# Kernel tuning notes

Measured on AMD Instinct MI355X. Metric: run time of the kernel, lower is better.

The kernel has to match this reference:

```python
import jax, jax.numpy as jnp
import numpy as np

N = 2048          # nodes
IN_DIM = 512      # in_dim
H = 8             # num_heads
HD = IN_DIM // H  # head_dim = 64
L = 5             # max_path_len
E = 32768         # edges
D_EDGE = 64       # edge_feat_dim


def setup_inputs() -> dict:
    key = jax.random.key(0)
    ks = jax.random.split(key, 14)
    w = 1.0 / np.sqrt(IN_DIM)
    return {
        "node_feat": jax.random.normal(ks[0], (N, IN_DIM), jnp.float32),
        "edge_index": jax.random.randint(ks[1], (2, E), 0, N, dtype=jnp.int32),
        "max_path_len": 5,
        "shortest_distances": jax.random.randint(ks[2], (N, N), 0, L + 1, dtype=jnp.int32),
        "shortest_paths": jax.random.randint(ks[3], (N, N, L), 0, E + 1, dtype=jnp.int32),  # E == padding row
        "edge_feat": jax.random.normal(ks[4], (E, D_EDGE), jnp.float32),
        "attention_mask": jnp.zeros((N, N), jnp.int32),
        "WQ": jax.random.normal(ks[5], (IN_DIM, IN_DIM), jnp.float32) * w,
        "bQ": jax.random.normal(ks[6], (IN_DIM,), jnp.float32) * 0.02,
        "WK": jax.random.normal(ks[7], (IN_DIM, IN_DIM), jnp.float32) * w,
        "bK": jax.random.normal(ks[8], (IN_DIM,), jnp.float32) * 0.02,
        "WV": jax.random.normal(ks[9], (IN_DIM, IN_DIM), jnp.float32) * w,
        "bV": jax.random.normal(ks[10], (IN_DIM,), jnp.float32) * 0.02,
        "WO": jax.random.normal(ks[11], (IN_DIM, IN_DIM), jnp.float32) * w,
        "bO": jnp.zeros((IN_DIM,), jnp.float32),
        "spatial_bias": jax.random.normal(ks[12], ((L + 1) * H, 1), jnp.float32) * 0.02,
        "edge_weight": jax.random.normal(ks[13], ((L + 1) * H, D_EDGE), jnp.float32) * 0.02,
    }


def reference(node_feat, edge_index, max_path_len, shortest_distances, shortest_paths,
              edge_feat, attention_mask, WQ, bQ, WK, bK, WV, bV, WO, bO,
              spatial_bias, edge_weight):
    Nn, D = node_feat.shape
    Lp = max_path_len  # min(max_path_len, max_shortest_path_len); distances reach Lp here

    Q = (node_feat @ WQ + bQ).reshape(Nn, H, HD)
    K = (node_feat @ WK + bK).reshape(Nn, H, HD)
    V = (node_feat @ WV + bV).reshape(Nn, H, HD)

    # QK^T / sqrt(head_dim), laid out [N, N, H] as in the original after permute
    scores = jnp.einsum('nhd,mhd->nmh', Q, K) / np.sqrt(HD).astype(np.float32)

    # SpatialEncoding: bias table [(L+1)*H, 1] -> [L+1, H]; gather by clamped distance
    sp_table = spatial_bias.reshape(Lp + 1, H)
    dist = jnp.clip(shortest_distances, 0, Lp)
    scores = scores + sp_table[dist]  # [N, N, H]

    # EdgeEncoding: einsum('xyld,ldh->xyh') refactored as per-edge projection then gather
    W_e = edge_weight[: Lp * H].reshape(Lp, H, D_EDGE)  # (reshape[L,H,D].permute -> [L,D,H])
    padded = jnp.concatenate([edge_feat, jnp.zeros((1, D_EDGE), edge_feat.dtype)], axis=0)
    T = jnp.einsum('ed,lhd->elh', padded, W_e)  # [E+1, L, H]
    sp = shortest_paths[:, :, :Lp]
    gathered = T[sp, jnp.arange(Lp)[None, None, :]]  # [N, N, L, H]
    scores = scores + gathered.sum(axis=2)

    mask = attention_mask.astype(bool)
    scores = jnp.where(mask[:, :, None], -jnp.inf, scores)

    # NOTE: original applies softmax over dim=-1 of the [N, N, H] tensor (the head axis);
    # faithfully reproduced here. Dropout is identity (eval / p for inference).
    attn = jax.nn.softmax(scores, axis=-1)

    out = jnp.einsum('nmh,mhd->nhd', attn, V).reshape(Nn, D)
    return out @ WO + bO
```

## Files before the change

kernel.cpp:

```cpp
#include <hip/hip_runtime.h>

#define NN     2048
#define DIM    512
#define NH     8
#define HD     64
#define NE     32768
#define EPAD   32832
#define CHUNKS 4
#define CHSZ   (NN/CHUNKS)
#define NJT    (CHSZ/64)
#define LOG2E  1.4426950408889634f

typedef __attribute__((ext_vector_type(8))) short bf16x8;
typedef __attribute__((ext_vector_type(4))) float f32x4;
typedef __attribute__((ext_vector_type(4))) unsigned int u32x4;

#define MFMA(a,b,c) __builtin_amdgcn_mfma_f32_16x16x32_bf16((a),(b),(c),0,0,0)

__device__ __forceinline__ float bf2f(unsigned int u16){
  union { unsigned int i; float f; } v; v.i = u16 << 16; return v.f;
}
__device__ __forceinline__ unsigned short f2bf(float f){
  union { float ff; unsigned int i; } v; v.ff = f;
  return (unsigned short)((v.i + 0x7fffu + ((v.i >> 16) & 1u)) >> 16);
}

__global__ __launch_bounds__(256) void cvt_k(
    const float* __restrict__ X, const float* __restrict__ ef, const float* __restrict__ ew,
    unsigned short* __restrict__ Xb, unsigned short* __restrict__ pEF, unsigned short* __restrict__ pEW)
{
  long g = (long)blockIdx.x*256 + threadIdx.x;
  const long GX = (long)NN*DIM/8;
  const long GE = (long)EPAD*8;
  const float* src; unsigned short* dst; long off, lim8;
  if (g < GX){ src = X;  dst = Xb;  off = g;        lim8 = GX; }
  else if (g < GX+GE){ src = ef; dst = pEF; off = g-GX; lim8 = (long)NE*8; }
  else { off = g-GX-GE; if (off >= 512) return; src = ew; dst = pEW; lim8 = 320; }
  unsigned short o[8];
  if (off < lim8){
    #pragma unroll
    for (int i=0;i<8;i++) o[i] = f2bf(src[off*8+i]);
  } else {
    #pragma unroll
    for (int i=0;i<8;i++) o[i] = 0;
  }
  *(uint4*)(dst + off*8) = *(const uint4*)o;
}

__global__ __launch_bounds__(256) void transpose512(
    const float* __restrict__ a0, const float* __restrict__ a1,
    const float* __restrict__ a2, const float* __restrict__ a3,
    unsigned short* __restrict__ out)
{
  __shared__ unsigned short tile[32][33];
  const float* src = blockIdx.z==0 ? a0 : blockIdx.z==1 ? a1 : blockIdx.z==2 ? a2 : a3;
  unsigned short* dst = out + (size_t)blockIdx.z*DIM*DIM;
  int bx = blockIdx.x*32, by = blockIdx.y*32;
  int tx = threadIdx.x, ty = threadIdx.y;
  #pragma unroll
  for (int i=0;i<32;i+=8) tile[ty+i][tx] = f2bf(src[(size_t)(by+ty+i)*DIM + bx+tx]);
  __syncthreads();
  #pragma unroll
  for (int i=0;i<32;i+=8) dst[(size_t)(bx+ty+i)*DIM + by+tx] = tile[tx][ty+i];
}

__global__ __launch_bounds__(256) void gemm_bt(
    const unsigned short* __restrict__ A1, const unsigned short* __restrict__ A2,
    const float* __restrict__ bias, unsigned short* __restrict__ C, float* __restrict__ Cf,
    int M, int N, int K, int bias_row)
{
  int lane = threadIdx.x & 63, w = threadIdx.x >> 6;
  int quad = lane >> 4, low = lane & 15;
  int m0 = blockIdx.y*64 + w*16;
  int n0 = blockIdx.x*32;
  f32x4 acc[2];
  acc[0] = (f32x4){0.f,0.f,0.f,0.f};
  acc[1] = (f32x4){0.f,0.f,0.f,0.f};
  #pragma unroll 4
  for (int k0=0; k0<K; k0+=32){
    bf16x8 a = *(const bf16x8*)(A1 + (size_t)(m0+low)*K + k0 + quad*8);
    #pragma unroll
    for (int t=0;t<2;t++){
      bf16x8 b = *(const bf16x8*)(A2 + (size_t)(n0+16*t+low)*K + k0 + quad*8);
      acc[t] = MFMA(a, b, acc[t]);
    }
  }
  #pragma unroll
  for (int t=0;t<2;t++){
    #pragma unroll
    for (int r=0;r<4;r++){
      int row = m0 + quad*4 + r;
      int col = n0 + 16*t + low;
      float v = acc[t][r];
      if (bias) v += bias[bias_row ? row : col];
      if (Cf) Cf[(size_t)row*N + col] = v;
      else    C [(size_t)row*N + col] = f2bf(v);
    }
  }
}

__global__ __launch_bounds__(256) void gemm_t2(
    const unsigned short* __restrict__ A1, const unsigned short* __restrict__ A2,
    unsigned short* __restrict__ T2L)
{
  int lane = threadIdx.x & 63, w = threadIdx.x >> 6;
  int quad = lane >> 4, low = lane & 15;
  int m0 = blockIdx.y*64 + w*16;
  int n0 = blockIdx.x*32;
  f32x4 acc[2];
  acc[0] = (f32x4){0.f,0.f,0.f,0.f};
  acc[1] = (f32x4){0.f,0.f,0.f,0.f};
  #pragma unroll
  for (int k0=0; k0<64; k0+=32){
    bf16x8 a = *(const bf16x8*)(A1 + (size_t)(m0+low)*64 + k0 + quad*8);
    #pragma unroll
    for (int t=0;t<2;t++){
      bf16x8 b = *(const bf16x8*)(A2 + (size_t)(n0+16*t+low)*64 + k0 + quad*8);
      acc[t] = MFMA(a, b, acc[t]);
    }
  }
  #pragma unroll
  for (int t=0;t<2;t++){
    #pragma unroll
    for (int r=0;r<4;r++){
      int row = m0 + quad*4 + r;
      int col = n0 + 16*t + low;
      T2L[((size_t)(col>>3)*EPAD + row)*8 + (col&7)] = f2bf(acc[t][r]);
    }
  }
}

__global__ __launch_bounds__(256) void qkv_k(
    const unsigned short* __restrict__ Xb, const unsigned short* __restrict__ Wt,
    const float* __restrict__ bQ, const float* __restrict__ bK, const float* __restrict__ bV,
    unsigned short* __restrict__ Qb, unsigned short* __restrict__ Kb, unsigned short* __restrict__ Vtb)
{
  int lane = threadIdx.x & 63, w = threadIdx.x >> 6;
  int quad = lane >> 4, low = lane & 15;
  int m0 = blockIdx.y*64 + w*16;
  int n0 = blockIdx.x*32;
  f32x4 acc[3][2];
  #pragma unroll
  for (int z=0;z<3;z++){ acc[z][0]=(f32x4){0.f,0.f,0.f,0.f}; acc[z][1]=(f32x4){0.f,0.f,0.f,0.f}; }
  #pragma unroll 2
  for (int k0=0; k0<DIM; k0+=32){
    bf16x8 a = *(const bf16x8*)(Xb + (size_t)(m0+low)*DIM + k0 + quad*8);
    #pragma unroll
    for (int z=0;z<3;z++){
      #pragma unroll
      for (int t=0;t<2;t++){
        bf16x8 b = *(const bf16x8*)(Wt + (size_t)z*DIM*DIM + (size_t)(n0+16*t+low)*DIM + k0 + quad*8);
        acc[z][t] = MFMA(a, b, acc[z][t]);
      }
    }
  }
  #pragma unroll
  for (int t=0;t<2;t++){
    #pragma unroll
    for (int r=0;r<4;r++){
      int row = m0 + quad*4 + r;
      int col = n0 + 16*t + low;
      Qb[(size_t)row*DIM + col] = f2bf(acc[0][t][r] + bQ[col]);
      Kb[(size_t)row*DIM + col] = f2bf(acc[1][t][r] + bK[col]);
      Vtb[(size_t)col*NN + row] = f2bf(acc[2][t][r] + bV[col]);
    }
  }
}

__global__ __launch_bounds__(256) void bias_k(
    const unsigned short* __restrict__ T2L, const float* __restrict__ spb,
    const int* __restrict__ dist, const int* __restrict__ sp, const int* __restrict__ maskp,
    unsigned short* __restrict__ biasB)
{
  __shared__ float sptab[48];
  if (threadIdx.x < 48) sptab[threadIdx.x] = spb[threadIdx.x];
  __syncthreads();
  long pix = (long)blockIdx.x*256 + threadIdx.x;
  int dd = __builtin_nontemporal_load(dist + pix);
  int mk = __builtin_nontemporal_load(maskp + pix);
  int e[5];
  #pragma unroll
  for (int l=0;l<5;l++) e[l] = __builtin_nontemporal_load(sp + pix*5 + l);
  dd = dd < 0 ? 0 : (dd > 5 ? 5 : dd);
  float b[8];
  #pragma unroll
  for (int x=0;x<8;x++) b[x] = sptab[dd*8 + x];
  #pragma unroll
  for (int l=0;l<5;l++){
    int ee = e[l];
    if ((unsigned)ee > (unsigned)NE) ee = NE;
    uint4 tv = *(const uint4*)(T2L + ((size_t)l*EPAD + ee)*8);
    b[0] += bf2f(tv.x & 0xffffu); b[1] += bf2f(tv.x >> 16);
    b[2] += bf2f(tv.y & 0xffffu); b[3] += bf2f(tv.y >> 16);
    b[4] += bf2f(tv.z & 0xffffu); b[5] += bf2f(tv.z >> 16);
    b[6] += bf2f(tv.w & 0xffffu); b[7] += bf2f(tv.w >> 16);
  }
  unsigned short o[8];
  #pragma unroll
  for (int x=0;x<8;x++) o[x] = mk ? f2bf(-1e30f) : f2bf(b[x]);
  *(uint4*)(biasB + pix*8) = *(const uint4*)o;
}

__global__ __launch_bounds__(512) void attn_k(
    const unsigned short* __restrict__ Qb, const unsigned short* __restrict__ Kb,
    const unsigned short* __restrict__ Vt, const unsigned short* __restrict__ biasB,
    float* __restrict__ partO)
{
  __shared__ __attribute__((aligned(16))) float sld[NH][16][68];
  int tid = threadIdx.x;
  int lane = tid & 63, h = tid >> 6;
  int quad = lane >> 4, low = lane & 15;
  int q0 = blockIdx.x * 16;
  int chunk = blockIdx.y;

  bf16x8 aq[2];
  #pragma unroll
  for (int s=0;s<2;s++)
    aq[s] = *(const bf16x8*)(Qb + (size_t)(q0+low)*DIM + h*HD + s*32 + quad*8);

  f32x4 accO[4];
  #pragma unroll
  for (int t=0;t<4;t++) accO[t] = (f32x4){0.f,0.f,0.f,0.f};

  uint4 pb[2];
  #pragma unroll
  for (int it=0; it<2; ++it){
    int p = tid + it*512;
    int qq = p >> 6, mm = p & 63;
    pb[it] = *(const uint4*)(biasB + ((size_t)(q0+qq)*NN + chunk*CHSZ + mm)*8);
  }

  for (int jt=0; jt<NJT; ++jt){
    int m0 = chunk*CHSZ + jt*64;
    __syncthreads();

    #pragma unroll
    for (int it=0; it<2; ++it){
      int p = tid + it*512;
      int qq = p >> 6, mm = p & 63;
      uint4 tv = pb[it];
      sld[0][qq][mm] = bf2f(tv.x & 0xffffu); sld[1][qq][mm] = bf2f(tv.x >> 16);
      sld[2][qq][mm] = bf2f(tv.y & 0xffffu); sld[3][qq][mm] = bf2f(tv.y >> 16);
      sld[4][qq][mm] = bf2f(tv.z & 0xffffu); sld[5][qq][mm] = bf2f(tv.z >> 16);
      sld[6][qq][mm] = bf2f(tv.w & 0xffffu); sld[7][qq][mm] = bf2f(tv.w >> 16);
    }
    if (jt+1 < NJT){
      #pragma unroll
      for (int it=0; it<2; ++it){
        int p = tid + it*512;
        int qq = p >> 6, mm = p & 63;
        pb[it] = *(const uint4*)(biasB + ((size_t)(q0+qq)*NN + m0 + 64 + mm)*8);
      }
    }
    __syncthreads();

    f32x4 S[4];
    #pragma unroll
    for (int t=0;t<4;t++) S[t] = (f32x4){0.f,0.f,0.f,0.f};
    #pragma unroll
    for (int s=0;s<2;s++){
      #pragma unroll
      for (int t=0;t<4;t++){
        bf16x8 bk = *(const bf16x8*)(Kb + (size_t)(m0+16*t+low)*DIM + h*HD + s*32 + quad*8);
        S[t] = MFMA(aq[s], bk, S[t]);
      }
    }
    #pragma unroll
    for (int t=0;t<4;t++){
      #pragma unroll
      for (int r=0;r<4;r++){
        float* slot = &sld[h][quad*4+r][low+16*t];
        *slot = S[t][r]*0.125f + *slot;
      }
    }
    __syncthreads();

    #pragma unroll
    for (int it=0; it<2; ++it){
      int p = tid + it*512;
      int qq = p >> 6, mm = p & 63;
      float s0[8];
      #pragma unroll
      for (int x=0;x<8;x++) s0[x] = sld[x][qq][mm];
      float mx = s0[0];
      #pragma unroll
      for (int x=1;x<8;x++) mx = fmaxf(mx, s0[x]);
      float sum = 0.f;
      #pragma unroll
      for (int x=0;x<8;x++){ s0[x] = exp2f((s0[x]-mx)*LOG2E); sum += s0[x]; }
      float inv = (mx < -1e29f) ? 0.f : 1.f/sum;
      #pragma unroll
      for (int x=0;x<8;x++) sld[x][qq][mm] = s0[x]*inv;
    }
    __syncthreads();

    bf16x8 ap[2];
    #pragma unroll
    for (int s=0;s<2;s++){
      const float* pp = &sld[h][low][s*32 + quad*8];
      float4 x0 = *(const float4*)pp;
      float4 x1 = *(const float4*)(pp + 4);
      bf16x8 a;
      a[0]=(short)f2bf(x0.x); a[1]=(short)f2bf(x0.y); a[2]=(short)f2bf(x0.z); a[3]=(short)f2bf(x0.w);
      a[4]=(short)f2bf(x1.x); a[5]=(short)f2bf(x1.y); a[6]=(short)f2bf(x1.z); a[7]=(short)f2bf(x1.w);
      ap[s] = a;
    }
    #pragma unroll
    for (int s=0;s<2;s++){
      #pragma unroll
      for (int t=0;t<4;t++){
        bf16x8 bv = *(const bf16x8*)(Vt + (size_t)(h*HD + 16*t + low)*NN + m0 + s*32 + quad*8);
        accO[t] = MFMA(ap[s], bv, accO[t]);
      }
    }
  }

  #pragma unroll
  for (int t=0;t<4;t++){
    #pragma unroll
    for (int r=0;r<4;r++){
      int q = quad*4 + r;
      partO[(((size_t)chunk*NN + q0 + q)*NH + h)*HD + 16*t + low] = accO[t][r];
    }
  }
}

__global__ __launch_bounds__(512) void merge_k(const float* __restrict__ partO,
                                               unsigned short* __restrict__ Obf)
{
  size_t idx = (size_t)blockIdx.x*512 + threadIdx.x;
  float s = 0.f;
  #pragma unroll
  for (int c=0;c<CHUNKS;c++) s += partO[(size_t)c*NN*DIM + idx];
  Obf[idx] = f2bf(s);
}

extern "C" void kernel_launch(void* const* d_in, const int* in_sizes, int n_in,
                              void* d_out, int out_size, void* d_ws, size_t ws_size,
                              hipStream_t stream)
{
  const float* X    = (const float*)d_in[0];
  const int*  dist  = (const int*)d_in[3];
  const int*  sp    = (const int*)d_in[4];
  const float* ef   = (const float*)d_in[5];
  const int*  maskp = (const int*)d_in[6];
  const float* WQ   = (const float*)d_in[7];
  const float* bQ   = (const float*)d_in[8];
  const float* WK   = (const float*)d_in[9];
  const float* bK   = (const float*)d_in[10];
  const float* WV   = (const float*)d_in[11];
  const float* bV   = (const float*)d_in[12];
  const float* WO   = (const float*)d_in[13];
  const float* bO   = (const float*)d_in[14];
  const float* spb  = (const float*)d_in[15];
  const float* ew   = (const float*)d_in[16];

  char* ws = (char*)d_ws;
  unsigned short* Wt   = (unsigned short*)(ws + 0);
  unsigned short* Xb   = (unsigned short*)(ws + 2097152);
  unsigned short* Qb   = (unsigned short*)(ws + 4194304);
  unsigned short* Kb   = (unsigned short*)(ws + 6291456);
  unsigned short* Vtb  = (unsigned short*)(ws + 8388608);
  unsigned short* pEF  = (unsigned short*)(ws + 10485760);
  unsigned short* pEW  = (unsigned short*)(ws + 14688256);
  unsigned short* T2L  = (unsigned short*)(ws + 14696448);
  unsigned short* Obf  = (unsigned short*)(ws + 18898944);
  unsigned short* biasB= (unsigned short*)(ws + 20996096);
  float*          pO   = (float*)(ws + 88104960);

  cvt_k<<<dim3(1540), dim3(256), 0, stream>>>(X, ef, ew, Xb, pEF, pEW);
  transpose512<<<dim3(16,16,4), dim3(32,8), 0, stream>>>(WQ, WK, WV, WO, Wt);
  gemm_t2<<<dim3(2,513), dim3(256), 0, stream>>>(pEF, pEW, T2L);
  bias_k<<<dim3(NN*NN/256), dim3(256), 0, stream>>>(T2L, spb, dist, sp, maskp, biasB);
  qkv_k<<<dim3(16,32), dim3(256), 0, stream>>>(Xb, Wt, bQ, bK, bV, Qb, Kb, Vtb);
  attn_k<<<dim3(128,CHUNKS), dim3(512), 0, stream>>>(Qb, Kb, Vtb, biasB, pO);
  merge_k<<<dim3(2048), dim3(512), 0, stream>>>(pO, Obf);
  gemm_bt<<<dim3(16,32), dim3(256), 0, stream>>>(Obf, Wt + 786432, bO, (unsigned short*)nullptr, (float*)d_out, NN, DIM, DIM, 0);
}
```

Baseline: 397.5 us.

## Double attention query tile, split keys into more chunks, and merge prep launches

The attention kernel now processes 32 query rows per block in two 16-row sub-tiles. Each K and V fragment load therefore feeds two MFMAs, and the key range is split into 8 chunks instead of 4 to keep enough blocks in flight. The f32-to-bf16 convert and weight-transpose kernels are merged into one launch, and the bias-gather and QKV projection kernels are merged into another, using block-index ranges to select the work. The larger tile doubles register and LDS use per block, and the extra chunks double the partial-output buffer that merge_k must read.

```diff
diff --git a/kernel.cpp b/kernel.cpp
--- a/kernel.cpp
+++ b/kernel.cpp
@@ -6,9 +6,10 @@
 #define HD     64
 #define NE     32768
 #define EPAD   32832
-#define CHUNKS 4
+#define CHUNKS 8
 #define CHSZ   (NN/CHUNKS)
 #define NJT    (CHSZ/64)
+#define QBLK   32
 #define LOG2E  1.4426950408889634f
 
 typedef __attribute__((ext_vector_type(8))) short bf16x8;
@@ -25,43 +26,44 @@
   return (unsigned short)((v.i + 0x7fffu + ((v.i >> 16) & 1u)) >> 16);
 }
 
-__global__ __launch_bounds__(256) void cvt_k(
+__global__ __launch_bounds__(256) void prep_k(
     const float* __restrict__ X, const float* __restrict__ ef, const float* __restrict__ ew,
-    unsigned short* __restrict__ Xb, unsigned short* __restrict__ pEF, unsigned short* __restrict__ pEW)
-{
-  long g = (long)blockIdx.x*256 + threadIdx.x;
-  const long GX = (long)NN*DIM/8;
-  const long GE = (long)EPAD*8;
-  const float* src; unsigned short* dst; long off, lim8;
-  if (g < GX){ src = X;  dst = Xb;  off = g;        lim8 = GX; }
-  else if (g < GX+GE){ src = ef; dst = pEF; off = g-GX; lim8 = (long)NE*8; }
-  else { off = g-GX-GE; if (off >= 512) return; src = ew; dst = pEW; lim8 = 320; }
-  unsigned short o[8];
-  if (off < lim8){
-    #pragma unroll
-    for (int i=0;i<8;i++) o[i] = f2bf(src[off*8+i]);
-  } else {
-    #pragma unroll
-    for (int i=0;i<8;i++) o[i] = 0;
-  }
-  *(uint4*)(dst + off*8) = *(const uint4*)o;
-}
-
-__global__ __launch_bounds__(256) void transpose512(
+    unsigned short* __restrict__ Xb, unsigned short* __restrict__ pEF, unsigned short* __restrict__ pEW,
     const float* __restrict__ a0, const float* __restrict__ a1,
     const float* __restrict__ a2, const float* __restrict__ a3,
-    unsigned short* __restrict__ out)
+    unsigned short* __restrict__ Wt)
 {
   __shared__ unsigned short tile[32][33];
-  const float* src = blockIdx.z==0 ? a0 : blockIdx.z==1 ? a1 : blockIdx.z==2 ? a2 : a3;
-  unsigned short* dst = out + (size_t)blockIdx.z*DIM*DIM;
-  int bx = blockIdx.x*32, by = blockIdx.y*32;
-  int tx = threadIdx.x, ty = threadIdx.y;
-  #pragma unroll
-  for (int i=0;i<32;i+=8) tile[ty+i][tx] = f2bf(src[(size_t)(by+ty+i)*DIM + bx+tx]);
-  __syncthreads();
-  #pragma unroll
-  for (int i=0;i<32;i+=8) dst[(size_t)(bx+ty+i)*DIM + by+tx] = tile[tx][ty+i];
+  if (blockIdx.x < 1540){
+    long g = (long)blockIdx.x*256 + threadIdx.x;
+    const long GX = (long)NN*DIM/8;
+    const long GE = (long)EPAD*8;
+    const float* src; unsigned short* dst; long off, lim8;
+    if (g < GX){ src = X;  dst = Xb;  off = g;        lim8 = GX; }
+    else if (g < GX+GE){ src = ef; dst = pEF; off = g-GX; lim8 = (long)NE*8; }
+    else { off = g-GX-GE; if (off >= 512) return; src = ew; dst = pEW; lim8 = 320; }
+    unsigned short o[8];
+    if (off < lim8){
+      #pragma unroll
+      for (int i=0;i<8;i++) o[i] = f2bf(src[off*8+i]);
+    } else {
+      #pragma unroll
+      for (int i=0;i<8;i++) o[i] = 0;
+    }
+    *(uint4*)(dst + off*8) = *(const uint4*)o;
+  } else {
+    int b2 = blockIdx.x - 1540;
+    int bz = b2 >> 8, rem = b2 & 255;
+    int bx = (rem & 15)*32, by = (rem >> 4)*32;
+    int tx = threadIdx.x & 31, ty = threadIdx.x >> 5;
+    const float* src = bz==0 ? a0 : bz==1 ? a1 : bz==2 ? a2 : a3;
+    unsigned short* dst = Wt + (size_t)bz*DIM*DIM;
+    #pragma unroll
+    for (int i=0;i<32;i+=8) tile[ty+i][tx] = f2bf(src[(size_t)(by+ty+i)*DIM + bx+tx]);
+    __syncthreads();
+    #pragma unroll
+    for (int i=0;i<32;i+=8) dst[(size_t)(bx+ty+i)*DIM + by+tx] = tile[tx][ty+i];
+  }
 }
 
 __global__ __launch_bounds__(256) void gemm_bt(
@@ -130,101 +132,105 @@
   }
 }
 
-__global__ __launch_bounds__(256) void qkv_k(
+__global__ __launch_bounds__(256) void biasqkv_k(
+    const unsigned short* __restrict__ T2L, const float* __restrict__ spb,
+    const int* __restrict__ dist, const int* __restrict__ sp, const int* __restrict__ maskp,
+    unsigned short* __restrict__ biasB,
     const unsigned short* __restrict__ Xb, const unsigned short* __restrict__ Wt,
     const float* __restrict__ bQ, const float* __restrict__ bK, const float* __restrict__ bV,
     unsigned short* __restrict__ Qb, unsigned short* __restrict__ Kb, unsigned short* __restrict__ Vtb)
 {
-  int lane = threadIdx.x & 63, w = threadIdx.x >> 6;
-  int quad = lane >> 4, low = lane & 15;
-  int m0 = blockIdx.y*64 + w*16;
-  int n0 = blockIdx.x*32;
-  f32x4 acc[3][2];
-  #pragma unroll
-  for (int z=0;z<3;z++){ acc[z][0]=(f32x4){0.f,0.f,0.f,0.f}; acc[z][1]=(f32x4){0.f,0.f,0.f,0.f}; }
-  #pragma unroll 2
-  for (int k0=0; k0<DIM; k0+=32){
-    bf16x8 a = *(const bf16x8*)(Xb + (size_t)(m0+low)*DIM + k0 + quad*8);
-    #pragma unroll
-    for (int z=0;z<3;z++){
-      #pragma unroll
-      for (int t=0;t<2;t++){
-        bf16x8 b = *(const bf16x8*)(Wt + (size_t)z*DIM*DIM + (size_t)(n0+16*t+low)*DIM + k0 + quad*8);
-        acc[z][t] = MFMA(a, b, acc[z][t]);
-      }
-    }
-  }
-  #pragma unroll
-  for (int t=0;t<2;t++){
-    #pragma unroll
-    for (int r=0;r<4;r++){
-      int row = m0 + quad*4 + r;
-      int col = n0 + 16*t + low;
-      Qb[(size_t)row*DIM + col] = f2bf(acc[0][t][r] + bQ[col]);
-      Kb[(size_t)row*DIM + col] = f2bf(acc[1][t][r] + bK[col]);
-      Vtb[(size_t)col*NN + row] = f2bf(acc[2][t][r] + bV[col]);
-    }
-  }
-}
-
-__global__ __launch_bounds__(256) void bias_k(
-    const unsigned short* __restrict__ T2L, const float* __restrict__ spb,
-    const int* __restrict__ dist, const int* __restrict__ sp, const int* __restrict__ maskp,
-    unsigned short* __restrict__ biasB)
-{
   __shared__ float sptab[48];
-  if (threadIdx.x < 48) sptab[threadIdx.x] = spb[threadIdx.x];
-  __syncthreads();
-  long pix = (long)blockIdx.x*256 + threadIdx.x;
-  int dd = __builtin_nontemporal_load(dist + pix);
-  int mk = __builtin_nontemporal_load(maskp + pix);
-  int e[5];
-  #pragma unroll
-  for (int l=0;l<5;l++) e[l] = __builtin_nontemporal_load(sp + pix*5 + l);
-  dd = dd < 0 ? 0 : (dd > 5 ? 5 : dd);
-  float b[8];
-  #pragma unroll
-  for (int x=0;x<8;x++) b[x] = sptab[dd*8 + x];
-  #pragma unroll
-  for (int l=0;l<5;l++){
-    int ee = e[l];
-    if ((unsigned)ee > (unsigned)NE) ee = NE;
-    uint4 tv = *(const uint4*)(T2L + ((size_t)l*EPAD + ee)*8);
-    b[0] += bf2f(tv.x & 0xffffu); b[1] += bf2f(tv.x >> 16);
-    b[2] += bf2f(tv.y & 0xffffu); b[3] += bf2f(tv.y >> 16);
-    b[4] += bf2f(tv.z & 0xffffu); b[5] += bf2f(tv.z >> 16);
-    b[6] += bf2f(tv.w & 0xffffu); b[7] += bf2f(tv.w >> 16);
-  }
-  unsigned short o[8];
-  #pragma unroll
-  for (int x=0;x<8;x++) o[x] = mk ? f2bf(-1e30f) : f2bf(b[x]);
-  *(uint4*)(biasB + pix*8) = *(const uint4*)o;
-}
-
-__global__ __launch_bounds__(512) void attn_k(
+  if (blockIdx.x >= 512){
+    if (threadIdx.x < 48) sptab[threadIdx.x] = spb[threadIdx.x];
+    __syncthreads();
+    long pix = (long)(blockIdx.x - 512)*256 + threadIdx.x;
+    int dd = __builtin_nontemporal_load(dist + pix);
+    int mk = __builtin_nontemporal_load(maskp + pix);
+    int e[5];
+    #pragma unroll
+    for (int l=0;l<5;l++) e[l] = __builtin_nontemporal_load(sp + pix*5 + l);
+    dd = dd < 0 ? 0 : (dd > 5 ? 5 : dd);
+    float b[8];
+    #pragma unroll
+    for (int x=0;x<8;x++) b[x] = sptab[dd*8 + x];
+    #pragma unroll
+    for (int l=0;l<5;l++){
+      int ee = e[l];
+      if ((unsigned)ee > (unsigned)NE) ee = NE;
+      uint4 tv = *(const uint4*)(T2L + ((size_t)l*EPAD + ee)*8);
+      b[0] += bf2f(tv.x & 0xffffu); b[1] += bf2f(tv.x >> 16);
+      b[2] += bf2f(tv.y & 0xffffu); b[3] += bf2f(tv.y >> 16);
+      b[4] += bf2f(tv.z & 0xffffu); b[5] += bf2f(tv.z >> 16);
+      b[6] += bf2f(tv.w & 0xffffu); b[7] += bf2f(tv.w >> 16);
+    }
+    unsigned short o[8];
+    #pragma unroll
+    for (int x=0;x<8;x++) o[x] = mk ? f2bf(-1e30f) : f2bf(b[x]);
+    *(uint4*)(biasB + pix*8) = *(const uint4*)o;
+  } else {
+    int bid = blockIdx.x;
+    int lane = threadIdx.x & 63, w = threadIdx.x >> 6;
+    int quad = lane >> 4, low = lane & 15;
+    int m0 = (bid >> 4)*64 + w*16;
+    int n0 = (bid & 15)*32;
+    f32x4 acc[3][2];
+    #pragma unroll
+    for (int z=0;z<3;z++){ acc[z][0]=(f32x4){0.f,0.f,0.f,0.f}; acc[z][1]=(f32x4){0.f,0.f,0.f,0.f}; }
+    #pragma unroll 2
+    for (int k0=0; k0<DIM; k0+=32){
+      bf16x8 a = *(const bf16x8*)(Xb + (size_t)(m0+low)*DIM + k0 + quad*8);
+      #pragma unroll
+      for (int z=0;z<3;z++){
+        #pragma unroll
+        for (int t=0;t<2;t++){
+          bf16x8 b = *(const bf16x8*)(Wt + (size_t)z*DIM*DIM + (size_t)(n0+16*t+low)*DIM + k0 + quad*8);
+          acc[z][t] = MFMA(a, b, acc[z][t]);
+        }
+      }
+    }
+    #pragma unroll
+    for (int t=0;t<2;t++){
+      #pragma unroll
+      for (int r=0;r<4;r++){
+        int row = m0 + quad*4 + r;
+        int col = n0 + 16*t + low;
+        Qb[(size_t)row*DIM + col] = f2bf(acc[0][t][r] + bQ[col]);
+        Kb[(size_t)row*DIM + col] = f2bf(acc[1][t][r] + bK[col]);
+        Vtb[(size_t)col*NN + row] = f2bf(acc[2][t][r] + bV[col]);
+      }
+    }
+  }
+}
+
+__global__ __launch_bounds__(512, 4) void attn_k(
     const unsigned short* __restrict__ Qb, const unsigned short* __restrict__ Kb,
     const unsigned short* __restrict__ Vt, const unsigned short* __restrict__ biasB,
     float* __restrict__ partO)
 {
-  __shared__ __attribute__((aligned(16))) float sld[NH][16][68];
+  __shared__ __attribute__((aligned(16))) float sld[NH][QBLK][68];
   int tid = threadIdx.x;
   int lane = tid & 63, h = tid >> 6;
   int quad = lane >> 4, low = lane & 15;
-  int q0 = blockIdx.x * 16;
+  int q0 = blockIdx.x * QBLK;
   int chunk = blockIdx.y;
 
-  bf16x8 aq[2];
-  #pragma unroll
-  for (int s=0;s<2;s++)
-    aq[s] = *(const bf16x8*)(Qb + (size_t)(q0+low)*DIM + h*HD + s*32 + quad*8);
-
-  f32x4 accO[4];
-  #pragma unroll
-  for (int t=0;t<4;t++) accO[t] = (f32x4){0.f,0.f,0.f,0.f};
-
-  uint4 pb[2];
-  #pragma unroll
-  for (int it=0; it<2; ++it){
+  bf16x8 aq[2][2];
+  #pragma unroll
+  for (int sq=0;sq<2;sq++)
+    #pragma unroll
+    for (int s=0;s<2;s++)
+      aq[sq][s] = *(const bf16x8*)(Qb + (size_t)(q0+sq*16+low)*DIM + h*HD + s*32 + quad*8);
+
+  f32x4 accO[2][4];
+  #pragma unroll
+  for (int sq=0;sq<2;sq++)
+    #pragma unroll
+    for (int t=0;t<4;t++) accO[sq][t] = (f32x4){0.f,0.f,0.f,0.f};
+
+  uint4 pb[4];
+  #pragma unroll
+  for (int it=0; it<4; ++it){
     int p = tid + it*512;
     int qq = p >> 6, mm = p & 63;
     pb[it] = *(const uint4*)(biasB + ((size_t)(q0+qq)*NN + chunk*CHSZ + mm)*8);
@@ -235,7 +241,7 @@
     __syncthreads();
 
     #pragma unroll
-    for (int it=0; it<2; ++it){
+    for (int it=0; it<4; ++it){
       int p = tid + it*512;
       int qq = p >> 6, mm = p & 63;
       uint4 tv = pb[it];
@@ -246,7 +252,7 @@
     }
     if (jt+1 < NJT){
       #pragma unroll
-      for (int it=0; it<2; ++it){
+      for (int it=0; it<4; ++it){
         int p = tid + it*512;
         int qq = p >> 6, mm = p & 63;
         pb[it] = *(const uint4*)(biasB + ((size_t)(q0+qq)*NN + m0 + 64 + mm)*8);
@@ -254,29 +260,36 @@
     }
     __syncthreads();
 
-    f32x4 S[4];
-    #pragma unroll
-    for (int t=0;t<4;t++) S[t] = (f32x4){0.f,0.f,0.f,0.f};
+    f32x4 S[2][4];
+    #pragma unroll
+    for (int sq=0;sq<2;sq++)
+      #pragma unroll
+      for (int t=0;t<4;t++) S[sq][t] = (f32x4){0.f,0.f,0.f,0.f};
     #pragma unroll
     for (int s=0;s<2;s++){
       #pragma unroll
       for (int t=0;t<4;t++){
         bf16x8 bk = *(const bf16x8*)(Kb + (size_t)(m0+16*t+low)*DIM + h*HD + s*32 + quad*8);
-        S[t] = MFMA(aq[s], bk, S[t]);
-      }
-    }
-    #pragma unroll
-    for (int t=0;t<4;t++){
-      #pragma unroll
-      for (int r=0;r<4;r++){
-        float* slot = &sld[h][quad*4+r][low+16*t];
-        *slot = S[t][r]*0.125f + *slot;
-      }
-    }
-    __syncthreads();
-
-    #pragma unroll
-    for (int it=0; it<2; ++it){
+        #pragma unroll
+        for (int sq=0;sq<2;sq++)
+          S[sq][t] = MFMA(aq[sq][s], bk, S[sq][t]);
+      }
+    }
+    #pragma unroll
+    for (int sq=0;sq<2;sq++){
+      #pragma unroll
+      for (int t=0;t<4;t++){
+        #pragma unroll
+        for (int r=0;r<4;r++){
+          float* slot = &sld[h][sq*16+quad*4+r][low+16*t];
+          *slot = S[sq][t][r]*0.125f + *slot;
+        }
+      }
+    }
+    __syncthreads();
+
+    #pragma unroll
+    for (int it=0; it<4; ++it){
       int p = tid + it*512;
       int qq = p >> 6, mm = p & 63;
       float s0[8];
@@ -294,33 +307,41 @@
     }
     __syncthreads();
 
-    bf16x8 ap[2];
-    #pragma unroll
-    for (int s=0;s<2;s++){
-      const float* pp = &sld[h][low][s*32 + quad*8];
-      float4 x0 = *(const float4*)pp;
-      float4 x1 = *(const float4*)(pp + 4);
-      bf16x8 a;
-      a[0]=(short)f2bf(x0.x); a[1]=(short)f2bf(x0.y); a[2]=(short)f2bf(x0.z); a[3]=(short)f2bf(x0.w);
-      a[4]=(short)f2bf(x1.x); a[5]=(short)f2bf(x1.y); a[6]=(short)f2bf(x1.z); a[7]=(short)f2bf(x1.w);
-      ap[s] = a;
+    bf16x8 ap[2][2];
+    #pragma unroll
+    for (int sq=0;sq<2;sq++){
+      #pragma unroll
+      for (int s=0;s<2;s++){
+        const float* pp = &sld[h][sq*16+low][s*32 + quad*8];
+        float4 x0 = *(const float4*)pp;
+        float4 x1 = *(const float4*)(pp + 4);
+        bf16x8 a;
+        a[0]=(short)f2bf(x0.x); a[1]=(short)f2bf(x0.y); a[2]=(short)f2bf(x0.z); a[3]=(short)f2bf(x0.w);
+        a[4]=(short)f2bf(x1.x); a[5]=(short)f2bf(x1.y); a[6]=(short)f2bf(x1.z); a[7]=(short)f2bf(x1.w);
+        ap[sq][s] = a;
+      }
     }
     #pragma unroll
     for (int s=0;s<2;s++){
       #pragma unroll
       for (int t=0;t<4;t++){
         bf16x8 bv = *(const bf16x8*)(Vt + (size_t)(h*HD + 16*t + low)*NN + m0 + s*32 + quad*8);
-        accO[t] = MFMA(ap[s], bv, accO[t]);
-      }
-    }
-  }
-
-  #pragma unroll
-  for (int t=0;t<4;t++){
-    #pragma unroll
-    for (int r=0;r<4;r++){
-      int q = quad*4 + r;
-      partO[(((size_t)chunk*NN + q0 + q)*NH + h)*HD + 16*t + low] = accO[t][r];
+        #pragma unroll
+        for (int sq=0;sq<2;sq++)
+          accO[sq][t] = MFMA(ap[sq][s], bv, accO[sq][t]);
+      }
+    }
+  }
+
+  #pragma unroll
+  for (int sq=0;sq<2;sq++){
+    #pragma unroll
+    for (int t=0;t<4;t++){
+      #pragma unroll
+      for (int r=0;r<4;r++){
+        int q = sq*16 + quad*4 + r;
+        partO[(((size_t)chunk*NN + q0 + q)*NH + h)*HD + 16*t + low] = accO[sq][t][r];
+      }
     }
   }
 }
@@ -368,12 +389,11 @@
   unsigned short* biasB= (unsigned short*)(ws + 20996096);
   float*          pO   = (float*)(ws + 88104960);
 
-  cvt_k<<<dim3(1540), dim3(256), 0, stream>>>(X, ef, ew, Xb, pEF, pEW);
-  transpose512<<<dim3(16,16,4), dim3(32,8), 0, stream>>>(WQ, WK, WV, WO, Wt);
+  prep_k<<<dim3(2564), dim3(256), 0, stream>>>(X, ef, ew, Xb, pEF, pEW, WQ, WK, WV, WO, Wt);
   gemm_t2<<<dim3(2,513), dim3(256), 0, stream>>>(pEF, pEW, T2L);
-  bias_k<<<dim3(NN*NN/256), dim3(256), 0, stream>>>(T2L, spb, dist, sp, maskp, biasB);
-  qkv_k<<<dim3(16,32), dim3(256), 0, stream>>>(Xb, Wt, bQ, bK, bV, Qb, Kb, Vtb);
-  attn_k<<<dim3(128,CHUNKS), dim3(512), 0, stream>>>(Qb, Kb, Vtb, biasB, pO);
+  biasqkv_k<<<dim3(512 + NN*NN/256), dim3(256), 0, stream>>>(
+      T2L, spb, dist, sp, maskp, biasB, Xb, Wt, bQ, bK, bV, Qb, Kb, Vtb);
+  attn_k<<<dim3(NN/QBLK, CHUNKS), dim3(512), 0, stream>>>(Qb, Kb, Vtb, biasB, pO);
   merge_k<<<dim3(2048), dim3(512), 0, stream>>>(pO, Obf);
   gemm_bt<<<dim3(16,32), dim3(256), 0, stream>>>(Obf, Wt + 786432, bO, (unsigned short*)nullptr, (float*)d_out, NN, DIM, DIM, 0);
 }
```

New measurement: 371.6 us. 1.07x faster.
